# Optimization experiments

Hardware: AMD Instinct MI355X
Metric: run time of the kernel (lower is better)

Reference implementation:

```python
import jax, jax.numpy as jnp
import numpy as np


def _pool2(t):
    # 2x2 max-pool + 2x2 avg-pool, summed. t: [B, C, H, W] with even H, W
    B, C, H, W = t.shape
    r = t.reshape(B, C, H // 2, 2, W // 2, 2)
    return r.max(axis=(3, 5)) + r.mean(axis=(3, 5))


def setup_inputs() -> dict:
    key = jax.random.key(0)
    k1, k2, k3, k4 = jax.random.split(key, 4)
    B, C, H, W = 32, 256, 56, 56
    x = jax.random.normal(k1, (B, C, H, W), dtype=jnp.float32)
    W1 = jax.random.normal(k2, (C // 2, C), dtype=jnp.float32) * 0.05
    W2 = jax.random.normal(k3, (C // 2, C), dtype=jnp.float32) * 0.05
    W3 = jax.random.normal(k4, (C, C), dtype=jnp.float32) * 0.05
    gamma = jnp.zeros((1,), dtype=jnp.float32)
    return {"x": x, "W1": W1, "W2": W2, "W3": W3, "gamma": gamma}


def reference(x, W1, W2, W3, gamma):
    B, C, H, W = x.shape
    # 1x1 convs (bias-free) == channel matmuls
    c1 = jnp.einsum('oc,bchw->bohw', W1, x)  # [B, C/2, H, W]
    c2 = jnp.einsum('oc,bchw->bohw', W2, x)  # [B, C/2, H, W]
    c3 = jnp.einsum('oc,bchw->bohw', W3, x)  # [B, C,   H, W]
    c1p = _pool2(c1)  # [B, C/2, H/2, W/2]
    c3p = _pool2(c3)  # [B, C,   H/2, W/2]
    n = H * W
    m = n // 4
    c1p_f = c1p.reshape(B, C // 2, m)
    c2_f = c2.reshape(B, C // 2, n)
    c3p_f = c3p.reshape(B, C, m)
    # matrix[b, n, m] = sum_c c2[b,c,n] * c1p[b,c,m]
    matrix = jnp.einsum('bcn,bcm->bnm', c2_f, c1p_f)
    attention = jax.nn.softmax(matrix, axis=-1)  # [B, n, m]
    # refined[b, c, n] = sum_m c3p[b,c,m] * attention[b,n,m]
    refined = jnp.einsum('bcm,bnm->bcn', c3p_f, attention).reshape(B, C, H, W)
    return gamma[0] * refined + x
```

## Files before the change

kernel.cpp:

```cpp
#include <hip/hip_runtime.h>

#define BATCH 32
#define CIN   256
#define CHALF 128
#define NPIX  3136
#define MPOOL 784
#define MPAD  896

typedef __bf16 bf16;
typedef __bf16 bf16x2 __attribute__((ext_vector_type(2)));
typedef __bf16 bf16x4 __attribute__((ext_vector_type(4)));
typedef __bf16 bf16x8 __attribute__((ext_vector_type(8)));
typedef float  f32x4  __attribute__((ext_vector_type(4)));

__global__ __launch_bounds__(256) void k_cast(
    const float* __restrict__ W1, const float* __restrict__ W2,
    const float* __restrict__ W3, bf16* __restrict__ Wcat)
{
    int u = blockIdx.x * 256 + threadIdx.x;
    int o = u >> 6, k4 = (u & 63) * 4;
    const float* src = (o < 128) ? (W1 + o * 256)
                     : (o < 256) ? (W2 + (o - 128) * 256)
                                 : (W3 + (o - 256) * 256);
    float4 v = *(const float4*)(src + k4);
    bf16x4 w = { (bf16)v.x, (bf16)v.y, (bf16)v.z, (bf16)v.w };
    *(bf16x4*)(Wcat + o * 256 + k4) = w;
}

#define XS_STRIDE   528
#define SLAB_STRIDE 520

__global__ __launch_bounds__(512) void k_conv(
    const float* __restrict__ x, const bf16* __restrict__ Wcat,
    bf16* __restrict__ c2n, bf16* __restrict__ c1pT, bf16* __restrict__ c3p)
{
    const int h2 = blockIdx.x, b = blockIdx.y;
    const int t = threadIdx.x;
    const int lane = t & 63, wave = t >> 6;
    const int l15 = lane & 15, lg = lane >> 4;

    __shared__ __align__(16) unsigned char smem[59136];

    if (h2 == 0) {
        float4 z = {0.f, 0.f, 0.f, 0.f};
        float4* p1 = (float4*)(c1pT + (size_t)b * MPAD * CHALF + (size_t)MPOOL * CHALF);
        for (int u = t; u < 1792; u += 512) p1[u] = z;
        bf16* p3 = c3p + (size_t)b * CIN * MPAD + MPOOL;
        for (int u = t; u < 256 * 14; u += 512) {
            int c = u / 14, g = u % 14;
            *(float4*)((char*)(p3 + (size_t)c * MPAD) + g * 16) = z;
        }
    }

    {
        const float* xb = x + (size_t)b * CIN * NPIX + h2 * 112;
        float vv[14][4];
        #pragma unroll
        for (int i = 0; i < 14; ++i) {
            int u = t + i * 512;
            int c4 = u / 112, n = u - c4 * 112;
            const float* s = xb + (size_t)(c4 * 4) * NPIX + n;
            vv[i][0] = s[0];
            vv[i][1] = s[NPIX];
            vv[i][2] = s[2 * NPIX];
            vv[i][3] = s[3 * NPIX];
        }
        #pragma unroll
        for (int i = 0; i < 14; ++i) {
            int u = t + i * 512;
            int c4 = u / 112, n = u - c4 * 112;
            bf16x4 w = {(bf16)vv[i][0], (bf16)vv[i][1], (bf16)vv[i][2], (bf16)vv[i][3]};
            *(bf16x4*)(smem + n * XS_STRIDE + c4 * 8) = w;
        }
    }
    __syncthreads();

    f32x4 acc[4][7];
    #pragma unroll
    for (int fo = 0; fo < 4; ++fo)
        #pragma unroll
        for (int fn = 0; fn < 7; ++fn) {
            f32x4 zz = {0.f, 0.f, 0.f, 0.f};
            acc[fo][fn] = zz;
        }
    {
        const int o0 = wave * 64;
        const bf16* wbase = Wcat + (size_t)(o0 + l15) * 256 + lg * 8;
        const unsigned char* xsb = smem + l15 * XS_STRIDE + lg * 16;
        #pragma unroll
        for (int ks = 0; ks < 8; ++ks) {
            bf16x8 afr[4], bfr[7];
            #pragma unroll
            for (int fo = 0; fo < 4; ++fo)
                afr[fo] = *(const bf16x8*)(wbase + fo * 16 * 256 + ks * 32);
            #pragma unroll
            for (int fn = 0; fn < 7; ++fn)
                bfr[fn] = *(const bf16x8*)(xsb + fn * 16 * XS_STRIDE + ks * 64);
            #pragma unroll
            for (int fo = 0; fo < 4; ++fo)
                #pragma unroll
                for (int fn = 0; fn < 7; ++fn)
                    acc[fo][fn] = __builtin_amdgcn_mfma_f32_16x16x32_bf16(
                        afr[fo], bfr[fn], acc[fo][fn], 0, 0, 0);
        }
    }

    __syncthreads();
    if (wave < 4) {
        #pragma unroll
        for (int fo = 0; fo < 4; ++fo)
            #pragma unroll
            for (int fn = 0; fn < 7; ++fn) {
                int n = fn * 16 + l15;
                int ol = wave * 64 + fo * 16 + lg * 4;
                f32x4 a = acc[fo][fn];
                bf16x4 w = {(bf16)a[0], (bf16)a[1], (bf16)a[2], (bf16)a[3]};
                *(bf16x4*)(smem + n * SLAB_STRIDE + ol * 2) = w;
            }
    }
    __syncthreads();
    {
        bf16* dst = c1pT + (size_t)b * MPAD * CHALF + (size_t)h2 * 28 * CHALF;
        for (int u = t; u < 896; u += 512) {
            int w2 = u >> 5, o4 = (u & 31) * 4;
            bf16x4 r0 = *(bf16x4*)(smem + (2 * w2)      * SLAB_STRIDE + o4 * 2);
            bf16x4 r1 = *(bf16x4*)(smem + (2 * w2 + 1)  * SLAB_STRIDE + o4 * 2);
            bf16x4 r2 = *(bf16x4*)(smem + (56 + 2 * w2) * SLAB_STRIDE + o4 * 2);
            bf16x4 r3 = *(bf16x4*)(smem + (57 + 2 * w2) * SLAB_STRIDE + o4 * 2);
            bf16x4 o_;
            #pragma unroll
            for (int j = 0; j < 4; ++j) {
                float p0 = (float)r0[j], p1 = (float)r1[j];
                float p2 = (float)r2[j], p3 = (float)r3[j];
                float mx = fmaxf(fmaxf(p0, p1), fmaxf(p2, p3));
                float av = (p0 + p1 + p2 + p3) * 0.25f;
                o_[j] = (bf16)(mx + av);
            }
            *(bf16x4*)(dst + (size_t)w2 * CHALF + o4) = o_;
        }
    }
    {
        bf16* dst = c2n + (size_t)b * NPIX * CHALF + (size_t)h2 * 112 * CHALF;
        for (int u = t; u < 3584; u += 512) {
            int n = u >> 5, o4 = (u & 31) * 4;
            bf16x4 v = *(bf16x4*)(smem + n * SLAB_STRIDE + 256 + o4 * 2);
            *(bf16x4*)(dst + (size_t)n * CHALF + o4) = v;
        }
    }

    __syncthreads();
    if (wave >= 4) {
        #pragma unroll
        for (int fo = 0; fo < 4; ++fo)
            #pragma unroll
            for (int fn = 0; fn < 7; ++fn) {
                int n = fn * 16 + l15;
                int ol = (wave - 4) * 64 + fo * 16 + lg * 4;
                f32x4 a = acc[fo][fn];
                bf16x4 w = {(bf16)a[0], (bf16)a[1], (bf16)a[2], (bf16)a[3]};
                *(bf16x4*)(smem + n * SLAB_STRIDE + ol * 2) = w;
            }
    }
    __syncthreads();
    {
        bf16* dst = c3p + (size_t)b * CIN * MPAD + h2 * 28;
        for (int u = t; u < 3584; u += 512) {
            int c = u / 14, w2p = u - c * 14;
            bf16x2 o_;
            #pragma unroll
            for (int k = 0; k < 2; ++k) {
                int w2 = 2 * w2p + k;
                float p0 = (float)*(bf16*)(smem + (2 * w2)      * SLAB_STRIDE + c * 2);
                float p1 = (float)*(bf16*)(smem + (2 * w2 + 1)  * SLAB_STRIDE + c * 2);
                float p2 = (float)*(bf16*)(smem + (56 + 2 * w2) * SLAB_STRIDE + c * 2);
                float p3 = (float)*(bf16*)(smem + (57 + 2 * w2) * SLAB_STRIDE + c * 2);
                float mx = fmaxf(fmaxf(p0, p1), fmaxf(p2, p3));
                float av = (p0 + p1 + p2 + p3) * 0.25f;
                o_[k] = (bf16)(mx + av);
            }
            *(bf16x2*)(dst + (size_t)c * MPAD + 2 * w2p) = o_;
        }
    }
}

#define STG_OFF 114688

__global__ __launch_bounds__(512) void k_attn(
    const bf16* __restrict__ c2n,
    const bf16* __restrict__ c1pT,
    const bf16* __restrict__ c3p,
    const float* __restrict__ x,
    const float* __restrict__ gamma,
    float* __restrict__ out)
{
    const int nb = blockIdx.x, b = blockIdx.y;
    const int n0 = nb * 64;
    const int t = threadIdx.x;
    const int lane = t & 63, wave = t >> 6;
    const int l15 = lane & 15, lg = lane >> 4;
    const int p = wave & 3, h = wave >> 2;

    __shared__ __align__(16) unsigned char smem[147456];
    unsigned char* stg = smem + STG_OFF;
    float* EX = (float*)stg;

    bf16x8 bq[4];
    {
        const bf16* c2b = c2n + ((size_t)b * NPIX + n0 + p * 16 + l15) * CHALF + lg * 8;
        #pragma unroll
        for (int k = 0; k < 4; ++k) bq[k] = *(const bf16x8*)(c2b + k * 32);
    }
    const bf16* c1b = c1pT + (size_t)b * MPAD * CHALF;
    const bf16* c3b = c3p + (size_t)b * CIN * MPAD;

    const int r0 = t >> 4, s0 = t & 15;
    const int cs = (s0 & 8) | ((s0 & 7) ^ (r0 & 7));
    const bf16* sA = c1b + (size_t)r0 * CHALF + cs * 8;
    const bf16* sB = c1b + (size_t)(448 + r0) * CHALF + cs * 8;

    uint4 rXa, rXb, rYa, rYb;
    rXa = *(const uint4*)(sA);
    rXb = *(const uint4*)(sB);
    *(uint4*)(stg + t * 16) = rXa;
    *(uint4*)(stg + 8192 + t * 16) = rXb;
    rYa = *(const uint4*)(sA + 4096);
    rYb = *(const uint4*)(sB + 4096);
    __syncthreads();

    f32x4 sacc[28];
    #pragma unroll
    for (int j = 0; j < 28; ++j) {
        f32x4 z = {0.f, 0.f, 0.f, 0.f};
        sacc[j] = z;
    }

    #pragma unroll
    for (int mc = 0; mc < 14; ++mc) {
        const unsigned char* bufc = stg + (mc & 1) * 16384;
        unsigned char* bufn = stg + ((mc & 1) ^ 1) * 16384;
        if (mc + 1 < 14) {
            if (mc & 1) { *(uint4*)(bufn + t * 16) = rXa; *(uint4*)(bufn + 8192 + t * 16) = rXb; }
            else        { *(uint4*)(bufn + t * 16) = rYa; *(uint4*)(bufn + 8192 + t * 16) = rYb; }
        }
        if (mc + 2 < 14) {
            if (mc & 1) { rYa = *(const uint4*)(sA + (mc + 2) * 4096); rYb = *(const uint4*)(sB + (mc + 2) * 4096); }
            else        { rXa = *(const uint4*)(sA + (mc + 2) * 4096); rXb = *(const uint4*)(sB + (mc + 2) * 4096); }
        }
        #pragma unroll
        for (int sf = 0; sf < 2; ++sf) {
            bf16x8 af[4];
            #pragma unroll
            for (int k = 0; k < 4; ++k)
                af[k] = *(const bf16x8*)(bufc + h * 8192 + (sf * 16 + l15) * 256
                                         + ((lg * 16 + k * 64) ^ ((l15 & 7) << 4)));
            #pragma unroll
            for (int k = 0; k < 4; ++k)
                sacc[mc * 2 + sf] = __builtin_amdgcn_mfma_f32_16x16x32_bf16(
                    af[k], bq[k], sacc[mc * 2 + sf], 0, 0, 0);
        }
        __syncthreads();
    }

    float mx = -1e30f;
    #pragma unroll
    for (int j = 0; j < 28; ++j) {
        if (h == 0 || j < 21)
            mx = fmaxf(mx, fmaxf(fmaxf(sacc[j][0], sacc[j][1]),
                                 fmaxf(sacc[j][2], sacc[j][3])));
    }
    mx = fmaxf(mx, __shfl_xor(mx, 16));
    mx = fmaxf(mx, __shfl_xor(mx, 32));
    if (lane < 16) EX[wave * 16 + l15] = mx;
    __syncthreads();
    mx = fmaxf(mx, EX[(wave ^ 4) * 16 + l15]);

    float s = 0.f;
    #pragma unroll
    for (int j = 0; j < 28; ++j) {
        if (h == 0 || j < 21) {
            #pragma unroll
            for (int r = 0; r < 4; ++r) {
                float e = __expf(sacc[j][r] - mx);
                sacc[j][r] = e;
                s += e;
            }
        }
    }
    s += __shfl_xor(s, 16);
    s += __shfl_xor(s, 32);
    if (lane < 16) EX[128 + wave * 16 + l15] = s;
    __syncthreads();
    s += EX[128 + (wave ^ 4) * 16 + l15];
    const float ri = 1.f / s;

    const int pc = t >> 2, ps = t & 3;
    const bf16* sV  = c3b + (size_t)pc * MPAD + ((ps ^ (pc & 3)) * 8);
    const bf16* sV2 = c3b + (size_t)(pc + 128) * MPAD + ((ps ^ (pc & 3)) * 8);
    rXa = *(const uint4*)(sV);
    rXb = *(const uint4*)(sV2);

    {
        const int n = p * 16 + l15;
        const unsigned sw = (unsigned)((n & 7) << 4);
        const unsigned rowb = (unsigned)(n * 1792);
        #pragma unroll
        for (int j = 0; j < 28; ++j) {
            bf16x4 w;
            if (h == 0 || j < 21) {
                w = bf16x4{ (bf16)(sacc[j][0] * ri), (bf16)(sacc[j][1] * ri),
                            (bf16)(sacc[j][2] * ri), (bf16)(sacc[j][3] * ri) };
            } else {
                w = bf16x4{ (bf16)0.f, (bf16)0.f, (bf16)0.f, (bf16)0.f };
            }
            unsigned byte = rowb + (unsigned)(h * 896 + j * 32 + lg * 8);
            *(bf16x4*)(smem + (byte ^ sw)) = w;
        }
    }
    __syncthreads();

    *(uint4*)(stg + t * 16) = rXa;
    *(uint4*)(stg + 8192 + t * 16) = rXb;
    rYa = *(const uint4*)(sV + 32);
    rYb = *(const uint4*)(sV2 + 32);
    __syncthreads();

    const int wn = h, wq = p;
    f32x4 acc2[2][4];
    #pragma unroll
    for (int fn = 0; fn < 2; ++fn)
        #pragma unroll
        for (int fc = 0; fc < 4; ++fc) {
            f32x4 z = {0.f, 0.f, 0.f, 0.f};
            acc2[fn][fc] = z;
        }

    #pragma unroll
    for (int ks = 0; ks < 28; ++ks) {
        const unsigned char* bufc = stg + (ks & 1) * 16384;
        unsigned char* bufn = stg + ((ks & 1) ^ 1) * 16384;
        if (ks + 1 < 28) {
            if (ks & 1) { *(uint4*)(bufn + t * 16) = rXa; *(uint4*)(bufn + 8192 + t * 16) = rXb; }
            else        { *(uint4*)(bufn + t * 16) = rYa; *(uint4*)(bufn + 8192 + t * 16) = rYb; }
        }
        if (ks + 2 < 28) {
            if (ks & 1) { rYa = *(const uint4*)(sV + (ks + 2) * 32); rYb = *(const uint4*)(sV2 + (ks + 2) * 32); }
            else        { rXa = *(const uint4*)(sV + (ks + 2) * 32); rXb = *(const uint4*)(sV2 + (ks + 2) * 32); }
        }
        {
            int nA0 = wn * 32 + l15, nA1 = nA0 + 16;
            int mb = (ks * 32 + lg * 8) * 2;
            bf16x8 af0 = *(const bf16x8*)(smem + ((nA0 * 1792 + mb) ^ ((nA0 & 7) << 4)));
            bf16x8 af1 = *(const bf16x8*)(smem + ((nA1 * 1792 + mb) ^ ((nA1 & 7) << 4)));
            #pragma unroll
            for (int fc = 0; fc < 4; ++fc) {
                int c = wq * 64 + fc * 16 + l15;
                bf16x8 bfr = *(const bf16x8*)(bufc + c * 64 + ((lg ^ (c & 3)) * 16));
                acc2[0][fc] = __builtin_amdgcn_mfma_f32_16x16x32_bf16(af0, bfr, acc2[0][fc], 0, 0, 0);
                acc2[1][fc] = __builtin_amdgcn_mfma_f32_16x16x32_bf16(af1, bfr, acc2[1][fc], 0, 0, 0);
            }
        }
        __syncthreads();
    }

    float* R = (float*)smem;
    #pragma unroll
    for (int fn = 0; fn < 2; ++fn)
        #pragma unroll
        for (int fc = 0; fc < 4; ++fc) {
            int c = wq * 64 + fc * 16 + l15;
            #pragma unroll
            for (int r = 0; r < 4; ++r) {
                int n = wn * 32 + fn * 16 + lg * 4 + r;
                R[n * 257 + c] = acc2[fn][fc][r];
            }
        }
    __syncthreads();
    const float g = gamma[0];
    const float* xb = x + (size_t)b * CIN * NPIX + n0;
    float* ob = out + (size_t)b * CIN * NPIX + n0;
    #pragma unroll 4
    for (int i = 0; i < 32; ++i) {
        int idx = t + i * 512;
        int c = idx >> 6, nn = idx & 63;
        size_t off = (size_t)c * NPIX + nn;
        ob[off] = g * R[nn * 257 + c] + xb[off];
    }
}

extern "C" void kernel_launch(void* const* d_in, const int* in_sizes, int n_in,
                              void* d_out, int out_size, void* d_ws, size_t ws_size,
                              hipStream_t stream) {
    const float* x     = (const float*)d_in[0];
    const float* W1    = (const float*)d_in[1];
    const float* W2    = (const float*)d_in[2];
    const float* W3    = (const float*)d_in[3];
    const float* gamma = (const float*)d_in[4];
    float* out = (float*)d_out;

    bf16* ws   = (bf16*)d_ws;
    bf16* Wcat = ws;
    bf16* c2n  = Wcat + (size_t)512 * 256;
    bf16* c1pT = c2n + (size_t)BATCH * NPIX * CHALF;
    bf16* c3p  = c1pT + (size_t)BATCH * MPAD * CHALF;

    k_cast<<<128, 256, 0, stream>>>(W1, W2, W3, Wcat);
    k_conv<<<dim3(28, BATCH), 512, 0, stream>>>(x, Wcat, c2n, c1pT, c3p);
    k_attn<<<dim3(49, BATCH), 512, 0, stream>>>(c2n, c1pT, c3p, x, gamma, out);
}
```

Measured before the change: 245.0 us.

## Load c3 B-fragments directly from global into registers, drop LDS staging

The second GEMM (attention times pooled c3) used to stage c3 tiles through a double-buffered LDS region, with a block-wide barrier every k-step. Each wave now loads its own B fragments straight from global memory into registers, software-pipelined two steps ahead, and all per-step __syncthreads are removed. This cuts barrier and LDS traffic. In exchange, c3 fragments are no longer shared across waves, so global/L2 reads go up, and the extra register buffers add pressure.

Result: slower. 337.3 us (+37.7%).

```diff
diff --git a/kernel.cpp b/kernel.cpp
--- a/kernel.cpp
+++ b/kernel.cpp
@@ -293,11 +293,14 @@
     s += EX[128 + (wave ^ 4) * 16 + l15];
     const float ri = 1.f / s;
 
-    const int pc = t >> 2, ps = t & 3;
-    const bf16* sV  = c3b + (size_t)pc * MPAD + ((ps ^ (pc & 3)) * 8);
-    const bf16* sV2 = c3b + (size_t)(pc + 128) * MPAD + ((ps ^ (pc & 3)) * 8);
-    rXa = *(const uint4*)(sV);
-    rXb = *(const uint4*)(sV2);
+    const int wn = h, wq = p;
+    const bf16* c3w = c3b + (size_t)(wq * 64 + l15) * MPAD + lg * 8;
+    bf16x8 v0[4], v1[4];
+    #pragma unroll
+    for (int fc = 0; fc < 4; ++fc) {
+        v0[fc] = *(const bf16x8*)(c3w + (size_t)fc * 16 * MPAD);
+        v1[fc] = *(const bf16x8*)(c3w + (size_t)fc * 16 * MPAD + 32);
+    }
 
     {
         const int n = p * 16 + l15;
@@ -318,13 +321,6 @@
     }
     __syncthreads();
 
-    *(uint4*)(stg + t * 16) = rXa;
-    *(uint4*)(stg + 8192 + t * 16) = rXb;
-    rYa = *(const uint4*)(sV + 32);
-    rYb = *(const uint4*)(sV2 + 32);
-    __syncthreads();
-
-    const int wn = h, wq = p;
     f32x4 acc2[2][4];
     #pragma unroll
     for (int fn = 0; fn < 2; ++fn)
@@ -334,34 +330,45 @@
             acc2[fn][fc] = z;
         }
 
-    #pragma unroll
-    for (int ks = 0; ks < 28; ++ks) {
-        const unsigned char* bufc = stg + (ks & 1) * 16384;
-        unsigned char* bufn = stg + ((ks & 1) ^ 1) * 16384;
-        if (ks + 1 < 28) {
-            if (ks & 1) { *(uint4*)(bufn + t * 16) = rXa; *(uint4*)(bufn + 8192 + t * 16) = rXb; }
-            else        { *(uint4*)(bufn + t * 16) = rYa; *(uint4*)(bufn + 8192 + t * 16) = rYb; }
+    const int nA0 = wn * 32 + l15, nA1 = nA0 + 16;
+    const unsigned swA0 = (unsigned)((nA0 & 7) << 4), swA1 = (unsigned)((nA1 & 7) << 4);
+    const unsigned rbA0 = (unsigned)(nA0 * 1792), rbA1 = (unsigned)(nA1 * 1792);
+
+    #pragma unroll
+    for (int ks = 0; ks < 28; ks += 2) {
+        {
+            unsigned mb = (unsigned)((ks * 32 + lg * 8) * 2);
+            bf16x8 af0 = *(const bf16x8*)(smem + ((rbA0 + mb) ^ swA0));
+            bf16x8 af1 = *(const bf16x8*)(smem + ((rbA1 + mb) ^ swA1));
+            #pragma unroll
+            for (int fc = 0; fc < 4; ++fc) {
+                acc2[0][fc] = __builtin_amdgcn_mfma_f32_16x16x32_bf16(af0, v0[fc], acc2[0][fc], 0, 0, 0);
+                acc2[1][fc] = __builtin_amdgcn_mfma_f32_16x16x32_bf16(af1, v0[fc], acc2[1][fc], 0, 0, 0);
+            }
         }
         if (ks + 2 < 28) {
-            if (ks & 1) { rYa = *(const uint4*)(sV + (ks + 2) * 32); rYb = *(const uint4*)(sV2 + (ks + 2) * 32); }
-            else        { rXa = *(const uint4*)(sV + (ks + 2) * 32); rXb = *(const uint4*)(sV2 + (ks + 2) * 32); }
+            #pragma unroll
+            for (int fc = 0; fc < 4; ++fc)
+                v0[fc] = *(const bf16x8*)(c3w + (size_t)fc * 16 * MPAD + (ks + 2) * 32);
         }
         {
-            int nA0 = wn * 32 + l15, nA1 = nA0 + 16;
-            int mb = (ks * 32 + lg * 8) * 2;
-            bf16x8 af0 = *(const bf16x8*)(smem + ((nA0 * 1792 + mb) ^ ((nA0 & 7) << 4)));
-            bf16x8 af1 = *(const bf16x8*)(smem + ((nA1 * 1792 + mb) ^ ((nA1 & 7) << 4)));
+            unsigned mb = (unsigned)(((ks + 1) * 32 + lg * 8) * 2);
+            bf16x8 af0 = *(const bf16x8*)(smem + ((rbA0 + mb) ^ swA0));
+            bf16x8 af1 = *(const bf16x8*)(smem + ((rbA1 + mb) ^ swA1));
             #pragma unroll
             for (int fc = 0; fc < 4; ++fc) {
-                int c = wq * 64 + fc * 16 + l15;
-                bf16x8 bfr = *(const bf16x8*)(bufc + c * 64 + ((lg ^ (c & 3)) * 16));
-                acc2[0][fc] = __builtin_amdgcn_mfma_f32_16x16x32_bf16(af0, bfr, acc2[0][fc], 0, 0, 0);
-                acc2[1][fc] = __builtin_amdgcn_mfma_f32_16x16x32_bf16(af1, bfr, acc2[1][fc], 0, 0, 0);
-            }
-        }
-        __syncthreads();
-    }
-
+                acc2[0][fc] = __builtin_amdgcn_mfma_f32_16x16x32_bf16(af0, v1[fc], acc2[0][fc], 0, 0, 0);
+                acc2[1][fc] = __builtin_amdgcn_mfma_f32_16x16x32_bf16(af1, v1[fc], acc2[1][fc], 0, 0, 0);
+            }
+        }
+        if (ks + 3 < 28) {
+            #pragma unroll
+            for (int fc = 0; fc < 4; ++fc)
+                v1[fc] = *(const bf16x8*)(c3w + (size_t)fc * 16 * MPAD + (ks + 3) * 32);
+        }
+    }
+
+    __syncthreads();
     float* R = (float*)smem;
     #pragma unroll
     for (int fn = 0; fn < 2; ++fn)
```

## Retile QK^T stage so each wave covers two n-fragments over interleaved m-tiles

Applied to the files above, without the earlier changes.

Reorganizes the score-computation phase of the attention kernel. Each wave now holds two 16-row query fragments and walks interleaved 16-column key tiles, so every loaded A fragment feeds two MFMAs. The key staging buffer grows to 128 rows per stage across 7 stages instead of 64 rows over 14. The softmax max and sum reductions now combine partials from four waves through shared memory instead of two. This cuts LDS reads per MFMA and halves the number of block barriers, at the cost of more registers and larger staging buffers.

After: 308.9 us. +26.1%, slower.

```diff
diff --git a/kernel.cpp b/kernel.cpp
--- a/kernel.cpp
+++ b/kernel.cpp
@@ -198,133 +198,194 @@
     const int t = threadIdx.x;
     const int lane = t & 63, wave = t >> 6;
     const int l15 = lane & 15, lg = lane >> 4;
-    const int p = wave & 3, h = wave >> 2;
+    const int ms = wave & 3, ng = wave >> 2;
 
     __shared__ __align__(16) unsigned char smem[147456];
     unsigned char* stg = smem + STG_OFF;
     float* EX = (float*)stg;
 
-    bf16x8 bq[4];
-    {
-        const bf16* c2b = c2n + ((size_t)b * NPIX + n0 + p * 16 + l15) * CHALF + lg * 8;
-        #pragma unroll
-        for (int k = 0; k < 4; ++k) bq[k] = *(const bf16x8*)(c2b + k * 32);
+    bf16x8 bq[2][4];
+    #pragma unroll
+    for (int nf = 0; nf < 2; ++nf) {
+        const bf16* c2b = c2n + ((size_t)b * NPIX + n0 + ng * 32 + nf * 16 + l15) * CHALF + lg * 8;
+        #pragma unroll
+        for (int k = 0; k < 4; ++k) bq[nf][k] = *(const bf16x8*)(c2b + k * 32);
     }
     const bf16* c1b = c1pT + (size_t)b * MPAD * CHALF;
     const bf16* c3b = c3p + (size_t)b * CIN * MPAD;
 
     const int r0 = t >> 4, s0 = t & 15;
     const int cs = (s0 & 8) | ((s0 & 7) ^ (r0 & 7));
-    const bf16* sA = c1b + (size_t)r0 * CHALF + cs * 8;
-    const bf16* sB = c1b + (size_t)(448 + r0) * CHALF + cs * 8;
-
-    uint4 rXa, rXb, rYa, rYb;
-    rXa = *(const uint4*)(sA);
-    rXb = *(const uint4*)(sB);
-    *(uint4*)(stg + t * 16) = rXa;
-    *(uint4*)(stg + 8192 + t * 16) = rXb;
-    rYa = *(const uint4*)(sA + 4096);
-    rYb = *(const uint4*)(sB + 4096);
-    __syncthreads();
-
-    f32x4 sacc[28];
-    #pragma unroll
-    for (int j = 0; j < 28; ++j) {
-        f32x4 z = {0.f, 0.f, 0.f, 0.f};
-        sacc[j] = z;
-    }
-
-    #pragma unroll
-    for (int mc = 0; mc < 14; ++mc) {
-        const unsigned char* bufc = stg + (mc & 1) * 16384;
-        unsigned char* bufn = stg + ((mc & 1) ^ 1) * 16384;
-        if (mc + 1 < 14) {
-            if (mc & 1) { *(uint4*)(bufn + t * 16) = rXa; *(uint4*)(bufn + 8192 + t * 16) = rXb; }
-            else        { *(uint4*)(bufn + t * 16) = rYa; *(uint4*)(bufn + 8192 + t * 16) = rYb; }
-        }
-        if (mc + 2 < 14) {
-            if (mc & 1) { rYa = *(const uint4*)(sA + (mc + 2) * 4096); rYb = *(const uint4*)(sB + (mc + 2) * 4096); }
-            else        { rXa = *(const uint4*)(sA + (mc + 2) * 4096); rXb = *(const uint4*)(sB + (mc + 2) * 4096); }
-        }
-        #pragma unroll
-        for (int sf = 0; sf < 2; ++sf) {
+    const bf16* sS = c1b + (size_t)r0 * CHALF + cs * 8;
+
+    uint4 rX[4], rY[4];
+    #pragma unroll
+    for (int i = 0; i < 4; ++i) rX[i] = *(const uint4*)(sS + (size_t)(i * 32) * CHALF);
+    #pragma unroll
+    for (int i = 0; i < 4; ++i) *(uint4*)(smem + (t + i * 512) * 16) = rX[i];
+    #pragma unroll
+    for (int i = 0; i < 4; ++i) rY[i] = *(const uint4*)(sS + (size_t)(128 + i * 32) * CHALF);
+    __syncthreads();
+
+    f32x4 sacc[7][2][2];
+    #pragma unroll
+    for (int c = 0; c < 7; ++c)
+        #pragma unroll
+        for (int mi = 0; mi < 2; ++mi)
+            #pragma unroll
+            for (int nf = 0; nf < 2; ++nf) {
+                f32x4 z = {0.f, 0.f, 0.f, 0.f};
+                sacc[c][mi][nf] = z;
+            }
+
+    #pragma unroll
+    for (int c = 0; c < 7; ++c) {
+        const unsigned char* bufc = smem + (c & 1) * 32768;
+        unsigned char* bufn = smem + ((c & 1) ^ 1) * 32768;
+        if (c + 1 < 7) {
+            if (c & 1) {
+                #pragma unroll
+                for (int i = 0; i < 4; ++i) *(uint4*)(bufn + (t + i * 512) * 16) = rX[i];
+            } else {
+                #pragma unroll
+                for (int i = 0; i < 4; ++i) *(uint4*)(bufn + (t + i * 512) * 16) = rY[i];
+            }
+        }
+        if (c + 2 < 7) {
+            if (c & 1) {
+                #pragma unroll
+                for (int i = 0; i < 4; ++i) rY[i] = *(const uint4*)(sS + (size_t)((c + 2) * 128 + i * 32) * CHALF);
+            } else {
+                #pragma unroll
+                for (int i = 0; i < 4; ++i) rX[i] = *(const uint4*)(sS + (size_t)((c + 2) * 128 + i * 32) * CHALF);
+            }
+        }
+        #pragma unroll
+        for (int mi = 0; mi < 2; ++mi) {
+            int mfl = ms + mi * 4;
             bf16x8 af[4];
             #pragma unroll
             for (int k = 0; k < 4; ++k)
-                af[k] = *(const bf16x8*)(bufc + h * 8192 + (sf * 16 + l15) * 256
+                af[k] = *(const bf16x8*)(bufc + (mfl * 16 + l15) * 256
                                          + ((lg * 16 + k * 64) ^ ((l15 & 7) << 4)));
             #pragma unroll
-            for (int k = 0; k < 4; ++k)
-                sacc[mc * 2 + sf] = __builtin_amdgcn_mfma_f32_16x16x32_bf16(
-                    af[k], bq[k], sacc[mc * 2 + sf], 0, 0, 0);
+            for (int k = 0; k < 4; ++k) {
+                sacc[c][mi][0] = __builtin_amdgcn_mfma_f32_16x16x32_bf16(af[k], bq[0][k], sacc[c][mi][0], 0, 0, 0);
+                sacc[c][mi][1] = __builtin_amdgcn_mfma_f32_16x16x32_bf16(af[k], bq[1][k], sacc[c][mi][1], 0, 0, 0);
+            }
         }
         __syncthreads();
     }
 
-    float mx = -1e30f;
-    #pragma unroll
-    for (int j = 0; j < 28; ++j) {
-        if (h == 0 || j < 21)
-            mx = fmaxf(mx, fmaxf(fmaxf(sacc[j][0], sacc[j][1]),
-                                 fmaxf(sacc[j][2], sacc[j][3])));
-    }
-    mx = fmaxf(mx, __shfl_xor(mx, 16));
-    mx = fmaxf(mx, __shfl_xor(mx, 32));
-    if (lane < 16) EX[wave * 16 + l15] = mx;
-    __syncthreads();
-    mx = fmaxf(mx, EX[(wave ^ 4) * 16 + l15]);
-
-    float s = 0.f;
-    #pragma unroll
-    for (int j = 0; j < 28; ++j) {
-        if (h == 0 || j < 21) {
-            #pragma unroll
-            for (int r = 0; r < 4; ++r) {
-                float e = __expf(sacc[j][r] - mx);
-                sacc[j][r] = e;
-                s += e;
-            }
-        }
-    }
-    s += __shfl_xor(s, 16);
-    s += __shfl_xor(s, 32);
-    if (lane < 16) EX[128 + wave * 16 + l15] = s;
-    __syncthreads();
-    s += EX[128 + (wave ^ 4) * 16 + l15];
-    const float ri = 1.f / s;
+    float mx[2] = { -1e30f, -1e30f };
+    #pragma unroll
+    for (int c = 0; c < 7; ++c)
+        #pragma unroll
+        for (int mi = 0; mi < 2; ++mi) {
+            if (c * 8 + 4 * mi + ms < 49) {
+                #pragma unroll
+                for (int nf = 0; nf < 2; ++nf) {
+                    f32x4 v = sacc[c][mi][nf];
+                    mx[nf] = fmaxf(mx[nf], fmaxf(fmaxf(v[0], v[1]), fmaxf(v[2], v[3])));
+                }
+            }
+        }
+    #pragma unroll
+    for (int nf = 0; nf < 2; ++nf) {
+        mx[nf] = fmaxf(mx[nf], __shfl_xor(mx[nf], 16));
+        mx[nf] = fmaxf(mx[nf], __shfl_xor(mx[nf], 32));
+    }
+    if (lane < 16) {
+        EX[(wave * 2 + 0) * 16 + l15] = mx[0];
+        EX[(wave * 2 + 1) * 16 + l15] = mx[1];
+    }
+    __syncthreads();
+    #pragma unroll
+    for (int nf = 0; nf < 2; ++nf) {
+        float m0 = EX[((ng * 4 + 0) * 2 + nf) * 16 + l15];
+        float m1 = EX[((ng * 4 + 1) * 2 + nf) * 16 + l15];
+        float m2 = EX[((ng * 4 + 2) * 2 + nf) * 16 + l15];
+        float m3 = EX[((ng * 4 + 3) * 2 + nf) * 16 + l15];
+        mx[nf] = fmaxf(fmaxf(m0, m1), fmaxf(m2, m3));
+    }
+
+    float sm[2] = { 0.f, 0.f };
+    #pragma unroll
+    for (int c = 0; c < 7; ++c)
+        #pragma unroll
+        for (int mi = 0; mi < 2; ++mi) {
+            if (c * 8 + 4 * mi + ms < 49) {
+                #pragma unroll
+                for (int nf = 0; nf < 2; ++nf) {
+                    #pragma unroll
+                    for (int r = 0; r < 4; ++r) {
+                        float e = __expf(sacc[c][mi][nf][r] - mx[nf]);
+                        sacc[c][mi][nf][r] = e;
+                        sm[nf] += e;
+                    }
+                }
+            }
+        }
+    #pragma unroll
+    for (int nf = 0; nf < 2; ++nf) {
+        sm[nf] += __shfl_xor(sm[nf], 16);
+        sm[nf] += __shfl_xor(sm[nf], 32);
+    }
+    if (lane < 16) {
+        EX[256 + (wave * 2 + 0) * 16 + l15] = sm[0];
+        EX[256 + (wave * 2 + 1) * 16 + l15] = sm[1];
+    }
+    __syncthreads();
+    float ri[2];
+    #pragma unroll
+    for (int nf = 0; nf < 2; ++nf) {
+        float s0v = EX[256 + ((ng * 4 + 0) * 2 + nf) * 16 + l15];
+        float s1v = EX[256 + ((ng * 4 + 1) * 2 + nf) * 16 + l15];
+        float s2v = EX[256 + ((ng * 4 + 2) * 2 + nf) * 16 + l15];
+        float s3v = EX[256 + ((ng * 4 + 3) * 2 + nf) * 16 + l15];
+        ri[nf] = 1.f / ((s0v + s1v) + (s2v + s3v));
+    }
 
     const int pc = t >> 2, ps = t & 3;
     const bf16* sV  = c3b + (size_t)pc * MPAD + ((ps ^ (pc & 3)) * 8);
     const bf16* sV2 = c3b + (size_t)(pc + 128) * MPAD + ((ps ^ (pc & 3)) * 8);
-    rXa = *(const uint4*)(sV);
-    rXb = *(const uint4*)(sV2);
-
-    {
-        const int n = p * 16 + l15;
-        const unsigned sw = (unsigned)((n & 7) << 4);
-        const unsigned rowb = (unsigned)(n * 1792);
-        #pragma unroll
-        for (int j = 0; j < 28; ++j) {
-            bf16x4 w;
-            if (h == 0 || j < 21) {
-                w = bf16x4{ (bf16)(sacc[j][0] * ri), (bf16)(sacc[j][1] * ri),
-                            (bf16)(sacc[j][2] * ri), (bf16)(sacc[j][3] * ri) };
-            } else {
-                w = bf16x4{ (bf16)0.f, (bf16)0.f, (bf16)0.f, (bf16)0.f };
-            }
-            unsigned byte = rowb + (unsigned)(h * 896 + j * 32 + lg * 8);
-            *(bf16x4*)(smem + (byte ^ sw)) = w;
-        }
+    uint4 rXa = *(const uint4*)(sV);
+    uint4 rXb = *(const uint4*)(sV2);
+
+    {
+        #pragma unroll
+        for (int c = 0; c < 7; ++c)
+            #pragma unroll
+            for (int mi = 0; mi < 2; ++mi) {
+                int gm = c * 8 + 4 * mi + ms;
+                bool valid = gm < 49;
+                #pragma unroll
+                for (int nf = 0; nf < 2; ++nf) {
+                    int n = ng * 32 + nf * 16 + l15;
+                    bf16x4 w;
+                    if (valid) {
+                        w = bf16x4{ (bf16)(sacc[c][mi][nf][0] * ri[nf]),
+                                    (bf16)(sacc[c][mi][nf][1] * ri[nf]),
+                                    (bf16)(sacc[c][mi][nf][2] * ri[nf]),
+                                    (bf16)(sacc[c][mi][nf][3] * ri[nf]) };
+                    } else {
+                        w = bf16x4{ (bf16)0.f, (bf16)0.f, (bf16)0.f, (bf16)0.f };
+                    }
+                    unsigned byte = (unsigned)(n * 1792 + gm * 32 + lg * 8)
+                                  ^ (unsigned)((n & 7) << 4);
+                    *(bf16x4*)(smem + byte) = w;
+                }
+            }
     }
     __syncthreads();
 
     *(uint4*)(stg + t * 16) = rXa;
     *(uint4*)(stg + 8192 + t * 16) = rXb;
-    rYa = *(const uint4*)(sV + 32);
-    rYb = *(const uint4*)(sV2 + 32);
-    __syncthreads();
-
-    const int wn = h, wq = p;
+    uint4 rYa = *(const uint4*)(sV + 32);
+    uint4 rYb = *(const uint4*)(sV2 + 32);
+    __syncthreads();
+
+    const int wn = ng, wq = ms;
     f32x4 acc2[2][4];
     #pragma unroll
     for (int fn = 0; fn < 2; ++fn)
```
